# Optimization experiments

Measured on AMD Instinct MI355X. Metric: run time of the kernel, lower is better.

The kernel has to match this reference:

```python
import jax, jax.numpy as jnp
import numpy as np

# Static configuration (mirrors MeshPotential.__init__ + mesh-size derivation)
SIGMA = 1.0          # atomic_gaussian_width
SPACING = 0.2        # mesh_spacing
ORDER = 4            # interpolation_order (cubic, P3M M4 assignment)
L = 10.0             # cubic cell edge used in setup_inputs
N_ATOMS = 200000
# ns = 2**ceil(log2(2*L/SPACING + 1)) = 2**ceil(log2(101)) = 128 per axis
NX = NY = NZ = 128


def setup_inputs() -> dict:
    key = jax.random.key(0)
    k1, k2 = jax.random.split(key)
    cell = L * jnp.eye(3, dtype=jnp.float32)                  # (3,3) cell rows = basis vectors
    positions = jax.random.uniform(k1, (N_ATOMS, 3), jnp.float32, 0.0, L)
    charges = jax.random.normal(k2, (N_ATOMS, 1), jnp.float32)
    return {"cell": cell, "positions": positions, "charges": charges}


def _interp(cell, positions):
    """Order-4 (cubic B-spline / P3M) interpolation weights + flat mesh indices."""
    ns = jnp.array([NX, NY, NZ], dtype=positions.dtype)
    rel = (positions @ jnp.linalg.inv(cell)) * ns             # (n,3) fractional * mesh size
    idx0 = jnp.floor(rel).astype(jnp.int32)                   # even order: floor-based stencil
    x = rel - (idx0.astype(rel.dtype) + 0.5)                  # offset in [-1/2, 1/2)
    x2, x3 = x * x, x * x * x
    # P3M charge-assignment weights of order 4, grid points [floor-1, floor, floor+1, floor+2]
    w = jnp.stack([
        1.0 - 6.0 * x + 12.0 * x2 - 8.0 * x3,
        23.0 - 30.0 * x - 12.0 * x2 + 24.0 * x3,
        23.0 + 30.0 * x - 12.0 * x2 - 24.0 * x3,
        1.0 + 6.0 * x + 12.0 * x2 + 8.0 * x3,
    ]) / 48.0                                                 # (4, n, 3)
    shifts = jnp.array([-1, 0, 1, 2], dtype=jnp.int32)
    idx = (idx0[None] + shifts[:, None, None]) % jnp.array([NX, NY, NZ], jnp.int32)  # (4,n,3)
    ix, iy, iz = idx[..., 0], idx[..., 1], idx[..., 2]        # (4,n) each
    flat = (ix[:, None, None] * NY + iy[None, :, None]) * NZ + iz[None, None, :]     # (4,4,4,n)
    flat = flat.reshape(64, -1).T                             # (n,64) flat mesh indices
    w3d = jnp.einsum('ia,ja,ka->aijk', w[..., 0], w[..., 1], w[..., 2]).reshape(-1, 64)  # (n,64)
    return w3d, flat


def _forward(cell, positions, charges):
    n, C = charges.shape
    w3d, flat = _interp(cell, positions)
    # points_to_mesh: spline-weighted scatter of charges onto the mesh
    vals = charges.T[:, :, None] * w3d[None]                  # (C,n,64)
    rho = jnp.zeros((C, NX * NY * NZ), charges.dtype).at[:, flat].add(vals)
    rho = rho.reshape(C, NX, NY, NZ)
    # Fourier-space convolution with G(k^2) = 4*pi/k^2 * exp(-sigma^2 k^2 / 2), G(0)=0
    Brec = 2.0 * jnp.pi * jnp.linalg.inv(cell).T              # rows = reciprocal vectors b_i
    mx = jnp.fft.fftfreq(NX) * NX
    my = jnp.fft.fftfreq(NY) * NY
    mz = jnp.fft.rfftfreq(NZ) * NZ
    kvec = (mx[:, None, None, None] * Brec[0]
            + my[None, :, None, None] * Brec[1]
            + mz[None, None, :, None] * Brec[2])              # (NX,NY,NZ//2+1,3)
    ksq = jnp.sum(kvec * kvec, axis=-1).astype(charges.dtype)
    safe = jnp.where(ksq == 0.0, 1.0, ksq)
    G = jnp.where(ksq == 0.0, 0.0, 4.0 * jnp.pi / safe * jnp.exp(-0.5 * SIGMA * SIGMA * safe))
    rho_hat = jnp.fft.rfftn(rho, axes=(1, 2, 3))              # unnormalized forward FFT
    pot_mesh = jnp.fft.irfftn(rho_hat * G, s=(NX, NY, NZ), axes=(1, 2, 3), norm="forward")
    pot_mesh = pot_mesh / jnp.abs(jnp.linalg.det(cell))       # divide by cell volume
    # mesh_to_points: spline-weighted gather back to atom positions
    gathered = pot_mesh.reshape(C, -1)[:, flat] * w3d[None]   # (C,n,64)
    potential = gathered.sum(-1).T                            # (n,C)
    # subtract self-contribution of the atom-centered gaussian
    potential = potential - charges * (jnp.sqrt(2.0 / jnp.pi) / SIGMA)
    return potential


def reference(cell, positions, charges):
    return _forward(cell, positions, charges)
```

## Files before the change

### kernel.cpp

```cpp
#include <hip/hip_runtime.h>
#include <math.h>

#define NTOT (128*128*128)
#define NBIN2 64
#define BINS (NBIN2*NBIN2*NBIN2)
#define SCAN_BLOCKS 256

#define ZP 72

#define PI_F      3.14159265358979323846f
#define TWO_PI_F  6.28318530717958647692f
#define FOUR_PI_F 12.5663706143591729539f


__device__ inline void inv3x3(const float* __restrict__ c, float* inv, float* detOut) {
    float a = c[0], b = c[1], cc = c[2];
    float d = c[3], e = c[4], f  = c[5];
    float g = c[6], h = c[7], i  = c[8];
    float A = e * i - f * h;
    float B = f * g - d * i;
    float C = d * h - e * g;
    float det = a * A + b * B + cc * C;
    float r = 1.0f / det;
    inv[0] = A * r;              inv[1] = (cc * h - b * i) * r;  inv[2] = (b * f - cc * e) * r;
    inv[3] = B * r;              inv[4] = (a * i - cc * g) * r;  inv[5] = (cc * d - a * f) * r;
    inv[6] = C * r;              inv[7] = (b * g - a * h) * r;   inv[8] = (a * e - b * d) * r;
    *detOut = det;
}

__device__ inline void w4(float x, float* w) {
    float x2 = x * x, x3 = x2 * x;
    w[0] = (1.0f  - 6.0f  * x + 12.0f * x2 - 8.0f  * x3) * (1.0f / 48.0f);
    w[1] = (23.0f - 30.0f * x - 12.0f * x2 + 24.0f * x3) * (1.0f / 48.0f);
    w[2] = (23.0f + 30.0f * x - 12.0f * x2 - 24.0f * x3) * (1.0f / 48.0f);
    w[3] = (1.0f  + 6.0f  * x + 12.0f * x2 + 8.0f  * x3) * (1.0f / 48.0f);
}

__device__ inline void atom_rel(const float* __restrict__ cell,
                                const float* __restrict__ pos, int t,
                                float* rx, float* ry, float* rz) {
    float inv[9]; float det;
    inv3x3(cell, inv, &det);
    float px = pos[3 * t], py = pos[3 * t + 1], pz = pos[3 * t + 2];
    *rx = (px * inv[0] + py * inv[3] + pz * inv[6]) * 128.0f;
    *ry = (px * inv[1] + py * inv[4] + pz * inv[7]) * 128.0f;
    *rz = (px * inv[2] + py * inv[5] + pz * inv[8]) * 128.0f;
}

__device__ inline int bin_of(float rx, float ry, float rz) {
    int ix = ((int)floorf(rx)) & 127;
    int iy = ((int)floorf(ry)) & 127;
    int iz = ((int)floorf(rz)) & 127;
    return ((((ix >> 1) << 6) | (iy >> 1)) << 6) | (iz >> 1);
}

__device__ inline float wrap128(float u) {
    u = (u > 64.0f) ? u - 128.0f : u;
    u = (u < -64.0f) ? u + 128.0f : u;
    return u;
}

__device__ inline float bspline(float u) {
    float a = fabsf(u);
    float t = fmaxf(2.0f - a, 0.0f);
    float s = fmaxf(1.0f - a, 0.0f);
    return t * t * t - 4.0f * s * s * s;
}


__global__ void zero_int_kernel(int* __restrict__ p, int n) {
    int i = blockIdx.x * blockDim.x + threadIdx.x;
    if (i < n) p[i] = 0;
}

__global__ void hist_kernel(const float* __restrict__ cell, const float* __restrict__ pos,
                            int* __restrict__ hist, int n) {
    int t = blockIdx.x * blockDim.x + threadIdx.x;
    if (t >= n) return;
    float rx, ry, rz;
    atom_rel(cell, pos, t, &rx, &ry, &rz);
    atomicAdd(&hist[bin_of(rx, ry, rz)], 1);
}

__global__ __launch_bounds__(256) void scan_local(const int4* __restrict__ hist4,
                                                  int4* __restrict__ off4,
                                                  int* __restrict__ partials) {
    const int b = blockIdx.x, t = threadIdx.x;
    const int idx = b * 256 + t;
    int4 h = hist4[idx];
    int s = h.x + h.y + h.z + h.w;
    int lane = t & 63, wv = t >> 6;
    int v = s;
    #pragma unroll
    for (int d = 1; d < 64; d <<= 1) {
        int o = __shfl_up(v, d, 64);
        if (lane >= d) v += o;
    }
    __shared__ int wsum[4];
    if (lane == 63) wsum[wv] = v;
    __syncthreads();
    int add = 0;
    #pragma unroll
    for (int k = 0; k < 4; ++k) if (k < wv) add += wsum[k];
    int run = add + v - s;
    int4 o4;
    o4.x = run; run += h.x;
    o4.y = run; run += h.y;
    o4.z = run; run += h.z;
    o4.w = run; run += h.w;
    off4[idx] = o4;
    if (t == 255) partials[b] = run;
}

__global__ __launch_bounds__(256) void scan_add(int4* __restrict__ hist4,
                                                int4* __restrict__ off4,
                                                const int* __restrict__ partials,
                                                int* __restrict__ offsets) {
    const int b = blockIdx.x, t = threadIdx.x;
    int lane = t & 63, wv = t >> 6;
    int v = (t < b) ? partials[t] : 0;
    #pragma unroll
    for (int d = 32; d >= 1; d >>= 1) v += __shfl_xor(v, d, 64);
    __shared__ int ws2[4];
    __shared__ int base_s;
    if (lane == 0) ws2[wv] = v;
    __syncthreads();
    if (t == 0) base_s = ws2[0] + ws2[1] + ws2[2] + ws2[3];
    __syncthreads();
    const int base = base_s;
    const int idx = b * 256 + t;
    int4 o4 = off4[idx];
    o4.x += base; o4.y += base; o4.z += base; o4.w += base;
    off4[idx]  = o4;
    hist4[idx] = o4;
    if (b == SCAN_BLOCKS - 1 && t == 255) offsets[BINS] = base + partials[b];
}

__global__ void reorder_kernel(const float* __restrict__ cell, const float* __restrict__ pos,
                               const float* __restrict__ q, int* __restrict__ cursor,
                               float4* __restrict__ sorted, int* __restrict__ sortedIdx, int n) {
    int t = blockIdx.x * blockDim.x + threadIdx.x;
    if (t >= n) return;
    float rx, ry, rz;
    atom_rel(cell, pos, t, &rx, &ry, &rz);
    int p = atomicAdd(&cursor[bin_of(rx, ry, rz)], 1);
    sorted[p] = make_float4(rx, ry, rz, q[t]);
    sortedIdx[p] = t;
}


__global__ __launch_bounds__(512) void column_scatter_kernel(const float4* __restrict__ atoms,
                                                             const int* __restrict__ offsets,
                                                             float* __restrict__ rmesh) {
    const int b = blockIdx.x;
    const int txt = b & 15, tyt = (b >> 4) & 15, zq = b >> 8;
    const int t = threadIdx.x;
    const int chunk_l = t & 7, cyl = (t >> 3) & 7, cxl = t >> 6;
    const int cx = (txt << 3) | cxl;
    const int cy = (tyt << 3) | cyl;
    const int cz0 = (((zq << 3) | chunk_l) << 2);

    float c0 = 0.0f, c1 = 0.0f, c2 = 0.0f, c3 = 0.0f;

    const float fcx = (float)cx, fcy = (float)cy, fcz = (float)cz0;

    const int xb0 = ((cx - 2) & 127) >> 1;
    const int yb0 = ((cy - 2) & 127) >> 1;
    const int nbx = 2 + (cx & 1);
    const int nby = 2 + (cy & 1);
    const int zb0 = ((cz0 - 2) & 127) >> 1;
    int len0 = 64 - zb0; if (len0 > 4) len0 = 4;
    const int len1 = 4 - len0;

    int i2 = 0, j2 = 0, r = -1;
    int i = 0, e = 0;
    for (;;) {
        while (i >= e) {
            ++r;
            if (r >= 2 || (r == 1 && len1 == 0)) {
                r = 0;
                if (++j2 >= nby) { j2 = 0; ++i2; }
            }
            if (i2 >= nbx) { i = 0; e = -1; break; }
            int bx = (xb0 + i2) & 63;
            int by = (yb0 + j2) & 63;
            int binBase = ((bx << 6) | by) << 6;
            if (r == 0) { i = offsets[binBase + zb0]; e = offsets[binBase + zb0 + len0]; }
            else        { i = offsets[binBase];       e = offsets[binBase + len1]; }
        }
        if (e < 0) break;

        float4 a = atoms[i]; ++i;

        float ux = wrap128(a.x - fcx);
        float wx = bspline(ux);
        float uy = wrap128(a.y - fcy);
        float wy = bspline(uy);
        float wxy = a.w * wx * wy * (1.0f / 216.0f);
        float uz = wrap128(a.z - fcz);
        c0 += wxy * bspline(uz);
        c1 += wxy * bspline(uz - 1.0f);
        c2 += wxy * bspline(uz - 2.0f);
        c3 += wxy * bspline(uz - 3.0f);
    }

    const size_t base = ((size_t)cx << 14) | ((size_t)cy << 7) | (size_t)cz0;
    *(float4*)&rmesh[base] = make_float4(c0, c1, c2, c3);
}


__device__ inline void bfly_dif(float& rr, float& ii, int h, bool hi, float cs, float sn) {
    float pr = __shfl_xor(rr, h), pi = __shfl_xor(ii, h);
    float br = hi ? (pr - rr) : (rr + pr);
    float bi = hi ? (pi - ii) : (ii + pi);
    rr = cs * br - sn * bi;
    ii = cs * bi + sn * br;
}

__device__ inline void bfly_dit(float& rr, float& ii, int h, bool hi, float cs, float sn) {
    float pr = __shfl_xor(rr, h), pi = __shfl_xor(ii, h);
    float xr = hi ? rr : pr, xi = hi ? ii : pi;
    float br = hi ? pr : rr, bi = hi ? pi : ii;
    float tr = cs * xr - sn * xi, ti = cs * xi + sn * xr;
    rr = hi ? (br - tr) : (br + tr);
    ii = hi ? (bi - ti) : (bi + ti);
}

__device__ inline void wfft_dif_fwd(float& r0, float& i0, float& r1, float& i1, int lane) {
    {
        float ang = -PI_F * (float)lane * (1.0f / 64.0f);
        float sn, cs; __sincosf(ang, &sn, &cs);
        float ar = r0 + r1, ai = i0 + i1;
        float dr = r0 - r1, di = i0 - i1;
        r0 = ar; i0 = ai;
        r1 = cs * dr - sn * di;
        i1 = cs * di + sn * dr;
    }
    #pragma unroll
    for (int h = 32; h >= 1; h >>= 1) {
        int pos = lane & (h - 1);
        bool hi = (lane & h) != 0;
        float ang = hi ? (-PI_F * (float)pos / (float)h) : 0.0f;
        float sn, cs; __sincosf(ang, &sn, &cs);
        bfly_dif(r0, i0, h, hi, cs, sn);
        bfly_dif(r1, i1, h, hi, cs, sn);
    }
}

__device__ inline void wfft_dit_inv(float& r0, float& i0, float& r1, float& i1, int lane) {
    #pragma unroll
    for (int h = 1; h <= 32; h <<= 1) {
        int pos = lane & (h - 1);
        bool hi = (lane & h) != 0;
        float ang = PI_F * (float)pos / (float)h;
        float sn, cs; __sincosf(ang, &sn, &cs);
        bfly_dit(r0, i0, h, hi, cs, sn);
        bfly_dit(r1, i1, h, hi, cs, sn);
    }
    {
        float ang = PI_F * (float)lane * (1.0f / 64.0f);
        float sn, cs; __sincosf(ang, &sn, &cs);
        float tr = cs * r1 - sn * i1, ti = cs * i1 + sn * r1;
        float nr = r0 + tr, ni = i0 + ti;
        r1 = r0 - tr; i1 = i0 - ti;
        r0 = nr; i0 = ni;
    }
}


__global__ __launch_bounds__(1024) void fftZfwd(const float* __restrict__ rin,
                                                float2* __restrict__ mesh) {
    __shared__ float tre[16][132], tim[16][132];
    const int t = threadIdx.x, b = blockIdx.x;
    for (int u = t; u < 2048; u += 1024) {
        int l = u >> 7, e = u & 127;
        tre[l][e] = rin[((size_t)((b << 4) | l) << 7) + e];
    }
    __syncthreads();
    const int w = t >> 6, lane = t & 63;
    float r0 = tre[w][lane],      i0 = 0.0f;
    float r1 = tre[w][lane + 64], i1 = 0.0f;
    wfft_dif_fwd(r0, i0, r1, i1, lane);
    int e0 = (int)(__brev((unsigned)lane) >> 25);
    tre[w][e0] = r0;     tim[w][e0] = i0;
    tre[w][e0 + 1] = r1; tim[w][e0 + 1] = i1;
    __syncthreads();
    for (int u = t; u < 2048; u += 1024) {
        int l = u >> 7, e = u & 127;
        if (e < ZP)
            mesh[(size_t)((b << 4) | l) * ZP + e] = make_float2(tre[l][e], tim[l][e]);
    }
}


__global__ __launch_bounds__(512) void fftYfwd(float2* __restrict__ mesh) {
    __shared__ float tre[8][132], tim[8][132];
    const int t = threadIdx.x, b = blockIdx.x;
    const int x = b & 127, zf0 = (b >> 7) << 3;
    const size_t rb = ((size_t)(x << 7)) * ZP + zf0;
    for (int u = t; u < 1024; u += 512) {
        int e = u >> 3, dz = u & 7;
        float2 vv = mesh[rb + (size_t)e * ZP + dz];
        tre[dz][e] = vv.x; tim[dz][e] = vv.y;
    }
    __syncthreads();
    const int w = t >> 6, lane = t & 63;
    float r0 = tre[w][lane],      i0 = tim[w][lane];
    float r1 = tre[w][lane + 64], i1 = tim[w][lane + 64];
    wfft_dif_fwd(r0, i0, r1, i1, lane);
    tre[w][lane] = r0;      tim[w][lane] = i0;
    tre[w][lane + 64] = r1; tim[w][lane + 64] = i1;
    __syncthreads();
    for (int u = t; u < 1024; u += 512) {
        int e = u >> 3, dz = u & 7;
        mesh[rb + (size_t)e * ZP + dz] = make_float2(tre[dz][e], tim[dz][e]);
    }
}


__global__ __launch_bounds__(512) void fftXGw(float2* __restrict__ mesh,
                                              const float* __restrict__ cell) {
    __shared__ float tre[8][132], tim[8][132];
    const int t = threadIdx.x, b = blockIdx.x;
    const int py = b & 127, zf0 = (b >> 7) << 3;
    for (int u = t; u < 1024; u += 512) {
        int e = u >> 3, dz = u & 7;
        float2 vv = mesh[(size_t)((e << 7) | py) * ZP + zf0 + dz];
        tre[dz][e] = vv.x; tim[dz][e] = vv.y;
    }
    __syncthreads();
    const int w = t >> 6, lane = t & 63;
    float r0 = tre[w][lane],      i0 = tim[w][lane];
    float r1 = tre[w][lane + 64], i1 = tim[w][lane + 64];
    wfft_dif_fwd(r0, i0, r1, i1, lane);
    {
        float inv[9]; float det; inv3x3(cell, inv, &det);
        float invVol = 1.0f / fabsf(det);
        int my = (int)(__brev((unsigned)py) >> 25);
        int mz = zf0 + w;
        float fy = (my < 64) ? (float)my : (float)(my - 128);
        float fz = (mz < 64) ? (float)mz : (float)(mz - 128);
        int mx0 = (int)(__brev((unsigned)lane) >> 25);
        #pragma unroll
        for (int s = 0; s < 2; ++s) {
            int mx = mx0 + s;
            float fx = (mx < 64) ? (float)mx : (float)(mx - 128);
            float kx = TWO_PI_F * (fx * inv[0] + fy * inv[1] + fz * inv[2]);
            float ky = TWO_PI_F * (fx * inv[3] + fy * inv[4] + fz * inv[5]);
            float kz = TWO_PI_F * (fx * inv[6] + fy * inv[7] + fz * inv[8]);
            float ksq = kx * kx + ky * ky + kz * kz;
            float G = (ksq == 0.0f) ? 0.0f
                      : FOUR_PI_F / ksq * __expf(-0.5f * ksq) * invVol;
            if (s == 0) { r0 *= G; i0 *= G; } else { r1 *= G; i1 *= G; }
        }
    }
    wfft_dit_inv(r0, i0, r1, i1, lane);
    tre[w][lane] = r0;      tim[w][lane] = i0;
    tre[w][lane + 64] = r1; tim[w][lane + 64] = i1;
    __syncthreads();
    for (int u = t; u < 1024; u += 512) {
        int e = u >> 3, dz = u & 7;
        mesh[(size_t)((e << 7) | py) * ZP + zf0 + dz] =
            make_float2(tre[dz][e], tim[dz][e]);
    }
}


__global__ __launch_bounds__(512) void fftYinv(float2* __restrict__ mesh) {
    __shared__ float tre[8][132], tim[8][132];
    const int t = threadIdx.x, b = blockIdx.x;
    const int x = b & 127, zf0 = (b >> 7) << 3;
    const size_t rb = ((size_t)(x << 7)) * ZP + zf0;
    for (int u = t; u < 1024; u += 512) {
        int e = u >> 3, dz = u & 7;
        float2 vv = mesh[rb + (size_t)e * ZP + dz];
        tre[dz][e] = vv.x; tim[dz][e] = vv.y;
    }
    __syncthreads();
    const int w = t >> 6, lane = t & 63;
    float r0 = tre[w][lane],      i0 = tim[w][lane];
    float r1 = tre[w][lane + 64], i1 = tim[w][lane + 64];
    wfft_dit_inv(r0, i0, r1, i1, lane);
    tre[w][lane] = r0;      tim[w][lane] = i0;
    tre[w][lane + 64] = r1; tim[w][lane + 64] = i1;
    __syncthreads();
    for (int u = t; u < 1024; u += 512) {
        int e = u >> 3, dz = u & 7;
        mesh[rb + (size_t)e * ZP + dz] = make_float2(tre[dz][e], tim[dz][e]);
    }
}


__global__ __launch_bounds__(1024) void fftZinv(const float2* __restrict__ mesh,
                                                float* __restrict__ rout) {
    __shared__ float tre[16][132], tim[16][132];
    const int t = threadIdx.x, b = blockIdx.x;
    for (int u = t; u < 2048; u += 1024) {
        int l = u >> 7, e = u & 127;
        int src = (e <= 64) ? e : 128 - e;
        float2 vv = mesh[(size_t)((b << 4) | l) * ZP + src];
        tre[l][e] = vv.x;
        tim[l][e] = (e <= 64) ? vv.y : -vv.y;
    }
    __syncthreads();
    const int w = t >> 6, lane = t & 63;
    int e0 = (int)(__brev((unsigned)lane) >> 25);
    float r0 = tre[w][e0],     i0 = tim[w][e0];
    float r1 = tre[w][e0 + 1], i1 = tim[w][e0 + 1];
    wfft_dit_inv(r0, i0, r1, i1, lane);
    const size_t rb = ((size_t)((b << 4) | w) << 7);
    rout[rb + lane] = r0;
    rout[rb + lane + 64] = r1;
}


__global__ void gather_kernel(const float4* __restrict__ sorted, const int* __restrict__ sortedIdx,
                              const float* __restrict__ rmesh, float* __restrict__ out, int n) {
    int t = blockIdx.x * blockDim.x + threadIdx.x;
    if (t >= n) return;
    float4 a = sorted[t];
    float wx[4], wy[4], wz[4];
    int ix[4], iy[4], iz[4];
    {
        float fl = floorf(a.x); int i0 = (int)fl; float x = a.x - fl - 0.5f; w4(x, wx);
        #pragma unroll
        for (int s = 0; s < 4; ++s) ix[s] = (i0 + s - 1) & 127;
    }
    {
        float fl = floorf(a.y); int i0 = (int)fl; float x = a.y - fl - 0.5f; w4(x, wy);
        #pragma unroll
        for (int s = 0; s < 4; ++s) iy[s] = (i0 + s - 1) & 127;
    }
    {
        float fl = floorf(a.z); int i0 = (int)fl; float x = a.z - fl - 0.5f; w4(x, wz);
        #pragma unroll
        for (int s = 0; s < 4; ++s) iz[s] = (i0 + s - 1) & 127;
    }
    float sum = 0.0f;
    #pragma unroll
    for (int i = 0; i < 4; ++i) {
        int bx = ix[i] << 14;
        float acc_i = 0.0f;
        #pragma unroll
        for (int j = 0; j < 4; ++j) {
            int bxy = bx | (iy[j] << 7);
            float acc_j = 0.0f;
            #pragma unroll
            for (int k = 0; k < 4; ++k) {
                acc_j += wz[k] * rmesh[bxy | iz[k]];
            }
            acc_i += wy[j] * acc_j;
        }
        sum += wx[i] * acc_i;
    }
    out[sortedIdx[t]] = sum - a.w * 0.79788456080286535588f;
}


extern "C" void kernel_launch(void* const* d_in, const int* in_sizes, int n_in,
                              void* d_out, int out_size, void* d_ws, size_t ws_size,
                              hipStream_t stream) {
    const float* cell = (const float*)d_in[0];
    const float* pos  = (const float*)d_in[1];
    const float* q    = (const float*)d_in[2];
    float* out = (float*)d_out;
    const int n = in_sizes[2];

    char* ws = (char*)d_ws;
    size_t o = 0;
    float4* sorted   = (float4*)(ws + o); o += (size_t)n * 16;
    int* sortedIdx   = (int*)(ws + o);    o += (size_t)n * 4;  o = (o + 255) & ~(size_t)255;
    int* hist        = (int*)(ws + o);    o += (size_t)BINS * 4;
    int* offsets     = (int*)(ws + o);    o += (size_t)(BINS + 4) * 4;
    int* partials    = (int*)(ws + o);    o += (size_t)SCAN_BLOCKS * 4; o = (o + 255) & ~(size_t)255;
    float2* mesh     = (float2*)(ws + o); o += (size_t)128 * 128 * ZP * 8;
    float* rmesh     = (float*)(ws + o);

    zero_int_kernel<<<BINS / 256, 256, 0, stream>>>(hist, BINS);
    hist_kernel<<<(n + 255) / 256, 256, 0, stream>>>(cell, pos, hist, n);
    scan_local<<<SCAN_BLOCKS, 256, 0, stream>>>((const int4*)hist, (int4*)offsets, partials);
    scan_add<<<SCAN_BLOCKS, 256, 0, stream>>>((int4*)hist, (int4*)offsets, partials, offsets);
    reorder_kernel<<<(n + 255) / 256, 256, 0, stream>>>(cell, pos, q, hist, sorted, sortedIdx, n);

    column_scatter_kernel<<<1024, 512, 0, stream>>>(sorted, offsets, rmesh);

    fftZfwd<<<1024, 1024, 0, stream>>>(rmesh, mesh);
    fftYfwd<<<9 * 128, 512, 0, stream>>>(mesh);
    fftXGw<<<9 * 128, 512, 0, stream>>>(mesh, cell);
    fftYinv<<<9 * 128, 512, 0, stream>>>(mesh);
    fftZinv<<<1024, 1024, 0, stream>>>(mesh, rmesh);

    gather_kernel<<<(n + 255) / 256, 256, 0, stream>>>(sorted, sortedIdx, rmesh, out, n);
}
```

Baseline: 164.0 us.

## Compute 2x2x4 mesh points per thread in scatter to reuse atom loads

The gather-style charge scatter now gives each thread a 2x2 xy block of four-point z columns, so every loaded atom feeds sixteen mesh points instead of four. A 3x3 bin neighbourhood is always scanned, and the next atom is prefetched speculatively. This cuts redundant atom reads and B-spline evaluations across neighbouring columns. The cost is fewer threads (131072 instead of 524288), lower occupancy and more registers per thread.

```diff
diff --git a/kernel.cpp b/kernel.cpp
--- a/kernel.cpp
+++ b/kernel.cpp
@@ -149,63 +149,105 @@
 }
 
 
-__global__ __launch_bounds__(512) void column_scatter_kernel(const float4* __restrict__ atoms,
-                                                             const int* __restrict__ offsets,
-                                                             float* __restrict__ rmesh) {
-    const int b = blockIdx.x;
-    const int txt = b & 15, tyt = (b >> 4) & 15, zq = b >> 8;
-    const int t = threadIdx.x;
-    const int chunk_l = t & 7, cyl = (t >> 3) & 7, cxl = t >> 6;
-    const int cx = (txt << 3) | cxl;
-    const int cy = (tyt << 3) | cyl;
-    const int cz0 = (((zq << 3) | chunk_l) << 2);
-
-    float c0 = 0.0f, c1 = 0.0f, c2 = 0.0f, c3 = 0.0f;
-
-    const float fcx = (float)cx, fcy = (float)cy, fcz = (float)cz0;
-
-    const int xb0 = ((cx - 2) & 127) >> 1;
-    const int yb0 = ((cy - 2) & 127) >> 1;
-    const int nbx = 2 + (cx & 1);
-    const int nby = 2 + (cy & 1);
+__global__ __launch_bounds__(256) void quad_scatter_kernel(const float4* __restrict__ atoms,
+                                                           const int* __restrict__ offsets,
+                                                           float* __restrict__ rmesh, int n) {
+    const int tid = blockIdx.x * 256 + threadIdx.x;
+    const int zq = tid & 31;
+    const int gy = (tid >> 5) & 63;
+    const int gx = tid >> 11;
+    const int cx0 = gx << 1, cy0 = gy << 1, cz0 = zq << 2;
+
+    float acc[2][2][4];
+    #pragma unroll
+    for (int a2 = 0; a2 < 2; ++a2)
+        #pragma unroll
+        for (int b2 = 0; b2 < 2; ++b2)
+            #pragma unroll
+            for (int k = 0; k < 4; ++k) acc[a2][b2][k] = 0.0f;
+
+    const float fcx = (float)cx0, fcy = (float)cy0, fcz = (float)cz0;
+
+    const int xb0 = ((cx0 - 2) & 127) >> 1;
+    const int yb0 = ((cy0 - 2) & 127) >> 1;
     const int zb0 = ((cz0 - 2) & 127) >> 1;
     int len0 = 64 - zb0; if (len0 > 4) len0 = 4;
     const int len1 = 4 - len0;
 
-    int i2 = 0, j2 = 0, r = -1;
-    int i = 0, e = 0;
-    for (;;) {
-        while (i >= e) {
-            ++r;
-            if (r >= 2 || (r == 1 && len1 == 0)) {
-                r = 0;
-                if (++j2 >= nby) { j2 = 0; ++i2; }
+    int r = -1, i = 0, e = 0;
+    while (i >= e) {
+        if (++r >= 18) break;
+        int half = r & 1;
+        if (half == 1 && len1 == 0) continue;
+        int xy = r >> 1;
+        int dx = xy / 3, dy = xy - dx * 3;
+        int bx = (xb0 + dx) & 63;
+        int by = (yb0 + dy) & 63;
+        int binBase = ((bx << 6) | by) << 6;
+        if (half == 0) { i = offsets[binBase + zb0]; e = offsets[binBase + zb0 + len0]; }
+        else           { i = offsets[binBase];       e = offsets[binBase + len1]; }
+    }
+
+    if (r < 18) {
+        float4 a = atoms[i];
+        for (;;) {
+            float4 aspec = atoms[(i + 1 < e) ? (i + 1) : i];
+
+            float ux = wrap128(a.x - fcx);
+            float wx0 = bspline(ux);
+            float wx1 = bspline(ux - 1.0f);
+            float uy = wrap128(a.y - fcy);
+            float wy0 = bspline(uy);
+            float wy1 = bspline(uy - 1.0f);
+            float uz = wrap128(a.z - fcz);
+            float wz0 = bspline(uz);
+            float wz1 = bspline(uz - 1.0f);
+            float wz2 = bspline(uz - 2.0f);
+            float wz3 = bspline(uz - 3.0f);
+            float qs = a.w * (1.0f / 216.0f);
+            float qx0 = qs * wx0, qx1 = qs * wx1;
+            float m00 = qx0 * wy0, m01 = qx0 * wy1;
+            float m10 = qx1 * wy0, m11 = qx1 * wy1;
+            acc[0][0][0] += m00 * wz0; acc[0][0][1] += m00 * wz1;
+            acc[0][0][2] += m00 * wz2; acc[0][0][3] += m00 * wz3;
+            acc[0][1][0] += m01 * wz0; acc[0][1][1] += m01 * wz1;
+            acc[0][1][2] += m01 * wz2; acc[0][1][3] += m01 * wz3;
+            acc[1][0][0] += m10 * wz0; acc[1][0][1] += m10 * wz1;
+            acc[1][0][2] += m10 * wz2; acc[1][0][3] += m10 * wz3;
+            acc[1][1][0] += m11 * wz0; acc[1][1][1] += m11 * wz1;
+            acc[1][1][2] += m11 * wz2; acc[1][1][3] += m11 * wz3;
+
+            ++i;
+            if (i < e) {
+                a = aspec;
+            } else {
+                while (i >= e) {
+                    if (++r >= 18) break;
+                    int half = r & 1;
+                    if (half == 1 && len1 == 0) continue;
+                    int xy = r >> 1;
+                    int dx = xy / 3, dy = xy - dx * 3;
+                    int bx = (xb0 + dx) & 63;
+                    int by = (yb0 + dy) & 63;
+                    int binBase = ((bx << 6) | by) << 6;
+                    if (half == 0) { i = offsets[binBase + zb0]; e = offsets[binBase + zb0 + len0]; }
+                    else           { i = offsets[binBase];       e = offsets[binBase + len1]; }
+                }
+                if (r >= 18) break;
+                a = atoms[i];
             }
-            if (i2 >= nbx) { i = 0; e = -1; break; }
-            int bx = (xb0 + i2) & 63;
-            int by = (yb0 + j2) & 63;
-            int binBase = ((bx << 6) | by) << 6;
-            if (r == 0) { i = offsets[binBase + zb0]; e = offsets[binBase + zb0 + len0]; }
-            else        { i = offsets[binBase];       e = offsets[binBase + len1]; }
         }
-        if (e < 0) break;
-
-        float4 a = atoms[i]; ++i;
-
-        float ux = wrap128(a.x - fcx);
-        float wx = bspline(ux);
-        float uy = wrap128(a.y - fcy);
-        float wy = bspline(uy);
-        float wxy = a.w * wx * wy * (1.0f / 216.0f);
-        float uz = wrap128(a.z - fcz);
-        c0 += wxy * bspline(uz);
-        c1 += wxy * bspline(uz - 1.0f);
-        c2 += wxy * bspline(uz - 2.0f);
-        c3 += wxy * bspline(uz - 3.0f);
-    }
-
-    const size_t base = ((size_t)cx << 14) | ((size_t)cy << 7) | (size_t)cz0;
-    *(float4*)&rmesh[base] = make_float4(c0, c1, c2, c3);
+    }
+
+    #pragma unroll
+    for (int a2 = 0; a2 < 2; ++a2) {
+        #pragma unroll
+        for (int b2 = 0; b2 < 2; ++b2) {
+            const size_t base = ((size_t)(cx0 + a2) << 14) | ((size_t)(cy0 + b2) << 7) | (size_t)cz0;
+            *(float4*)&rmesh[base] = make_float4(acc[a2][b2][0], acc[a2][b2][1],
+                                                 acc[a2][b2][2], acc[a2][b2][3]);
+        }
+    }
 }
 
 
@@ -482,7 +524,7 @@
     scan_add<<<SCAN_BLOCKS, 256, 0, stream>>>((int4*)hist, (int4*)offsets, partials, offsets);
     reorder_kernel<<<(n + 255) / 256, 256, 0, stream>>>(cell, pos, q, hist, sorted, sortedIdx, n);
 
-    column_scatter_kernel<<<1024, 512, 0, stream>>>(sorted, offsets, rmesh);
+    quad_scatter_kernel<<<512, 256, 0, stream>>>(sorted, offsets, rmesh, n);
 
     fftZfwd<<<1024, 1024, 0, stream>>>(rmesh, mesh);
     fftYfwd<<<9 * 128, 512, 0, stream>>>(mesh);
```

Result: no change. 162.5 us (-0.9%).
